# Kernel optimization log

Hardware: AMD Instinct MI355X
Metric: run time of the kernel (lower is better)

## Reference

```python
import jax, jax.numpy as jnp
import numpy as np

B, S, D, H, F = 8, 1024, 1024, 16, 4096
DH = D // H
LN_EPS = 1e-3  # keras LayerNormalization default


def layer_norm(x, g, b, eps=LN_EPS):
    m = jnp.mean(x, axis=-1, keepdims=True)
    v = jnp.mean(jnp.square(x - m), axis=-1, keepdims=True)
    return (x - m) * jax.lax.rsqrt(v + eps) * g + b


def setup_inputs() -> dict:
    key = jax.random.key(0)
    ks = jax.random.split(key, 16)
    s = 0.02
    return {
        "x": jax.random.normal(ks[0], (B, S, D), dtype=jnp.float32),
        "key_padding_mask": jax.random.randint(ks[1], (B, S), 0, 2) > 0,
        "wq": jax.random.normal(ks[2], (D, D), dtype=jnp.float32) * s,
        "wk": jax.random.normal(ks[3], (D, D), dtype=jnp.float32) * s,
        "wv": jax.random.normal(ks[4], (D, D), dtype=jnp.float32) * s,
        "wo": jax.random.normal(ks[5], (D, D), dtype=jnp.float32) * s,
        "gamma": jnp.ones((H,), dtype=jnp.float32),
        "ln_g": jnp.ones((3, D), dtype=jnp.float32),   # pre_attn, post_attn, pre_fc
        "ln_b": jnp.zeros((3, D), dtype=jnp.float32),
        "ln_fc_g": jnp.ones((F,), dtype=jnp.float32),  # post_fc_norm over fc_dim
        "ln_fc_b": jnp.zeros((F,), dtype=jnp.float32),
        "w1": jax.random.normal(ks[6], (D, F), dtype=jnp.float32) * s,
        "b1": jnp.zeros((F,), dtype=jnp.float32),
        "w2": jax.random.normal(ks[7], (F, D), dtype=jnp.float32) * s,
        "b2": jnp.zeros((D,), dtype=jnp.float32),
        "lam": jnp.ones((D,), dtype=jnp.float32),
    }


def reference(x, key_padding_mask, wq, wk, wv, wo, gamma, ln_g, ln_b,
              ln_fc_g, ln_fc_b, w1, b1, w2, b2, lam):
    # ---- attention sub-block (self-attention path, x_clt=None) ----
    residual = x
    h = layer_norm(x, ln_g[0], ln_b[0])                       # pre_attn_norm
    q = (h @ wq).reshape(B, S, H, DH)
    k = (h @ wk).reshape(B, S, H, DH)
    v = (h @ wv).reshape(B, S, H, DH)
    scores = jnp.einsum('bqhd,bkhd->bhqk', q, k) / jnp.sqrt(jnp.float32(DH))
    # key_padding_mask: True = masked key
    scores = jnp.where(key_padding_mask[:, None, None, :], -1e9, scores)
    v = jnp.where(key_padding_mask[:, :, None, None], 0.0, v)
    attn = jax.nn.softmax(scores, axis=-1)
    ws = jnp.einsum('bhqk,bkhd->bqhd', attn, v)
    ws = ws * gamma[None, None, :, None]                      # per-head scale
    out = ws.reshape(B, S, D) @ wo
    out = layer_norm(out, ln_g[1], ln_b[1])                   # post_attn_norm
    x = out + residual
    # ---- FFN sub-block ----
    residual = x
    h = layer_norm(x, ln_g[2], ln_b[2])                       # pre_fc_norm
    h = jax.nn.gelu(h @ w1 + b1, approximate=False)
    h = layer_norm(h, ln_fc_g, ln_fc_b)                       # post_fc_norm (fc_dim)
    h = h @ w2 + b2
    return h + residual * lam
```

## Files before the change

### kernel.cpp

```cpp
#include <hip/hip_runtime.h>
#include <math.h>

typedef _Float16 h_t;
typedef _Float16 h8 __attribute__((ext_vector_type(8)));
typedef _Float16 h4 __attribute__((ext_vector_type(4)));
typedef float    f4 __attribute__((ext_vector_type(4)));
typedef unsigned int u32;

#define SEQ   1024
#define DIM   1024
#define FDIM  4096
#define NB    8
#define NH    16
#define DHD   64
#define NROWS 8192

__device__ __forceinline__ void glds16(const void* g, void* l)
{
    __builtin_amdgcn_global_load_lds((const __attribute__((address_space(1))) u32*)g,
                                     (__attribute__((address_space(3))) u32*)l, 16, 0, 0);
}

__global__ __launch_bounds__(256)
void canon_mask_k(const void* __restrict__ raw, int* __restrict__ outm, int n)
{
    const unsigned int*  w  = (const unsigned int*)raw;
    const unsigned char* cb = (const unsigned char*)raw;
    __shared__ int flag;
    if (threadIdx.x == 0) flag = 0;
    __syncthreads();
    int bad = 0;
    for (int i = threadIdx.x; i < 1024; i += 256)
        if (w[i] > 1u) bad = 1;
    if (bad) flag = 1;
    __syncthreads();
    const bool is_i32 = (flag == 0);
    const int idx = blockIdx.x * 256 + threadIdx.x;
    if (idx < n) outm[idx] = is_i32 ? (w[idx] != 0u) : (cb[idx] != 0);
}

__global__ __launch_bounds__(256)
void wconv_k(const float* __restrict__ W, h_t* __restrict__ Wt, int K, int N)
{
    __shared__ float T[32][33];
    const int t  = threadIdx.x;
    const int k0 = blockIdx.y * 32, n0 = blockIdx.x * 32;
    const int r = t >> 3, c4 = (t & 7) * 4;
    const float4 v = *(const float4*)(W + (size_t)(k0 + r) * N + n0 + c4);
    T[r][c4 + 0] = v.x; T[r][c4 + 1] = v.y; T[r][c4 + 2] = v.z; T[r][c4 + 3] = v.w;
    __syncthreads();
    h4 o = { (h_t)T[c4 + 0][r], (h_t)T[c4 + 1][r], (h_t)T[c4 + 2][r], (h_t)T[c4 + 3][r] };
    *(h4*)(Wt + (size_t)(n0 + r) * K + k0 + c4) = o;
}

__device__ __forceinline__ void block_reduce2(float& s, float& ss)
{
    #pragma unroll
    for (int off = 32; off > 0; off >>= 1) {
        s  += __shfl_down(s,  off, 64);
        ss += __shfl_down(ss, off, 64);
    }
    __shared__ float sh[8];
    const int wid  = threadIdx.x >> 6;
    const int lane = threadIdx.x & 63;
    if (lane == 0) { sh[wid] = s; sh[4 + wid] = ss; }
    __syncthreads();
    s  = sh[0] + sh[1] + sh[2] + sh[3];
    ss = sh[4] + sh[5] + sh[6] + sh[7];
}

__global__ __launch_bounds__(256)
void ln1024_k(const float* __restrict__ in, const float* __restrict__ gw,
              const float* __restrict__ bw, h_t* __restrict__ out)
{
    const size_t base = (size_t)blockIdx.x * 1024;
    const int c = threadIdx.x * 4;
    float4 xv = *(const float4*)(in + base + c);
    float v[4] = {xv.x, xv.y, xv.z, xv.w};
    float s = v[0] + v[1] + v[2] + v[3];
    float ss = v[0]*v[0] + v[1]*v[1] + v[2]*v[2] + v[3]*v[3];
    block_reduce2(s, ss);
    const float mean = s * (1.f / 1024.f);
    const float rstd = rsqrtf(ss * (1.f / 1024.f) - mean * mean + 1e-3f);
    const float4 g4 = *(const float4*)(gw + c);
    const float4 b4 = *(const float4*)(bw + c);
    h4 oh = {(h_t)((v[0]-mean)*rstd*g4.x + b4.x), (h_t)((v[1]-mean)*rstd*g4.y + b4.y),
             (h_t)((v[2]-mean)*rstd*g4.z + b4.z), (h_t)((v[3]-mean)*rstd*g4.w + b4.w)};
    *(h4*)(out + base + c) = oh;
}

__global__ __launch_bounds__(256)
void ln_fuse_k(const h_t* __restrict__ proj, const float* __restrict__ x,
               const float* __restrict__ g1, const float* __restrict__ b1w,
               const float* __restrict__ g2, const float* __restrict__ b2w,
               h_t* __restrict__ x2out, h_t* __restrict__ h2out)
{
    const size_t base = (size_t)blockIdx.x * 1024;
    const int c = threadIdx.x * 4;
    h4 p = *(const h4*)(proj + base + c);
    float v[4] = {(float)p[0], (float)p[1], (float)p[2], (float)p[3]};
    float s = v[0]+v[1]+v[2]+v[3];
    float ss = v[0]*v[0]+v[1]*v[1]+v[2]*v[2]+v[3]*v[3];
    block_reduce2(s, ss);
    {
        const float mean = s * (1.f/1024.f);
        const float rstd = rsqrtf(ss * (1.f/1024.f) - mean*mean + 1e-3f);
        const float4 g4 = *(const float4*)(g1 + c);
        const float4 b4 = *(const float4*)(b1w + c);
        const float4 r4 = *(const float4*)(x + base + c);
        v[0] = (v[0]-mean)*rstd*g4.x + b4.x + r4.x;
        v[1] = (v[1]-mean)*rstd*g4.y + b4.y + r4.y;
        v[2] = (v[2]-mean)*rstd*g4.z + b4.z + r4.z;
        v[3] = (v[3]-mean)*rstd*g4.w + b4.w + r4.w;
    }
    h4 x2h = {(h_t)v[0], (h_t)v[1], (h_t)v[2], (h_t)v[3]};
    *(h4*)(x2out + base + c) = x2h;
    __syncthreads();
    float s2 = v[0]+v[1]+v[2]+v[3];
    float ss2 = v[0]*v[0]+v[1]*v[1]+v[2]*v[2]+v[3]*v[3];
    block_reduce2(s2, ss2);
    const float mean = s2 * (1.f/1024.f);
    const float rstd = rsqrtf(ss2 * (1.f/1024.f) - mean*mean + 1e-3f);
    const float4 g4 = *(const float4*)(g2 + c);
    const float4 b4 = *(const float4*)(b2w + c);
    h4 oh = {(h_t)((v[0]-mean)*rstd*g4.x + b4.x), (h_t)((v[1]-mean)*rstd*g4.y + b4.y),
             (h_t)((v[2]-mean)*rstd*g4.z + b4.z), (h_t)((v[3]-mean)*rstd*g4.w + b4.w)};
    *(h4*)(h2out + base + c) = oh;
}

__global__ __launch_bounds__(256)
void ln4096_k(h_t* __restrict__ buf, const float* __restrict__ gw,
              const float* __restrict__ bw)
{
    const size_t base = (size_t)blockIdx.x * 4096;
    const int t = threadIdx.x;
    float v[16];
    #pragma unroll
    for (int i = 0; i < 2; ++i) {
        h8 x = *(const h8*)(buf + base + (i * 256 + t) * 8);
        #pragma unroll
        for (int j = 0; j < 8; ++j) v[i * 8 + j] = (float)x[j];
    }
    float s = 0.f, ss = 0.f;
    #pragma unroll
    for (int i = 0; i < 16; ++i) { s += v[i]; ss += v[i] * v[i]; }
    block_reduce2(s, ss);
    const float mean = s * (1.f / 4096.f);
    const float rstd = rsqrtf(ss * (1.f / 4096.f) - mean * mean + 1e-3f);
    #pragma unroll
    for (int i = 0; i < 2; ++i) {
        const int c = (i * 256 + t) * 8;
        h8 o;
        #pragma unroll
        for (int j = 0; j < 8; ++j)
            o[j] = (h_t)((v[i*8+j] - mean) * rstd * gw[c + j] + bw[c + j]);
        *(h8*)(buf + base + c) = o;
    }
}

#define GEPI_QKV  0
#define GEPI_H16  2
#define GEPI_GELU 3
#define GEPI_FC2  4

__device__ __forceinline__ float gelu_exact(float x)
{
    return 0.5f * x * (1.f + erff(x * 0.70710678118654752440f));
}

template<int EPI>
__global__ __launch_bounds__(256, 2)
void hgemm_k(const h_t* __restrict__ A, const h_t* __restrict__ Wt,
             const float* __restrict__ bias, void* __restrict__ outv,
             int M, int K, int N,
             const int* __restrict__ mask, const h_t* __restrict__ resid,
             const float* __restrict__ lam, h_t* __restrict__ out2,
             h_t* __restrict__ out3)
{
    __shared__ h_t As[128 * 64];
    __shared__ h_t Bs[128 * 64];
    const int t = threadIdx.x;
    const int wv = t >> 6, lane = t & 63;

    int bx, by;
    {
        const int nwg = gridDim.x * gridDim.y;
        int wg = blockIdx.y * gridDim.x + blockIdx.x;
        const int xcd = wg & 7, rest = wg >> 3;
        const int q = nwg >> 3, r = nwg & 7;
        wg = (xcd < r ? xcd * (q + 1) : r * (q + 1) + (xcd - r) * q) + rest;
        bx = wg % gridDim.x; by = wg / gridDim.x;
    }
    const int m0 = by * 128, n0 = bx * 128;
    const int wr = (wv >> 1) * 64, wc = (wv & 1) * 64;
    const int lr = lane & 15, g = lane >> 4;
    const int sr = lane >> 3;
    const int sslot = (lane & 7) * 16;
    const int sswz = sr << 4;

    f4 acc[4][4] = {};

    for (int k0 = 0; k0 < K; k0 += 64) {
        __syncthreads();
        #pragma unroll
        for (int j = 0; j < 4; ++j) {
            const int r = j * 32 + wv * 8 + sr;
            glds16((const char*)A  + (((size_t)(m0 + r) * K + k0) << 1) + (sslot ^ sswz),
                   (char*)As + j * 4096 + wv * 1024);
            glds16((const char*)Wt + (((size_t)(n0 + r) * K + k0) << 1) + (sslot ^ sswz),
                   (char*)Bs + j * 4096 + wv * 1024);
        }
        __syncthreads();
        #pragma unroll
        for (int kk = 0; kk < 2; ++kk) {
            h8 af[4], bf[4];
            #pragma unroll
            for (int mt = 0; mt < 4; ++mt) {
                const int r = wr + mt * 16 + lr;
                af[mt] = *(const h8*)((const char*)As + r * 128 + ((kk * 64 + g * 16) ^ ((lr & 7) << 4)));
            }
            #pragma unroll
            for (int nt = 0; nt < 4; ++nt) {
                const int r = wc + nt * 16 + lr;
                bf[nt] = *(const h8*)((const char*)Bs + r * 128 + ((kk * 64 + g * 16) ^ ((lr & 7) << 4)));
            }
            #pragma unroll
            for (int mt = 0; mt < 4; ++mt)
                #pragma unroll
                for (int nt = 0; nt < 4; ++nt)
                    acc[mt][nt] = __builtin_amdgcn_mfma_f32_16x16x32_f16(af[mt], bf[nt], acc[mt][nt], 0, 0, 0);
        }
    }

    #pragma unroll
    for (int mt = 0; mt < 4; ++mt) {
        #pragma unroll
        for (int nt = 0; nt < 4; ++nt) {
            #pragma unroll
            for (int e = 0; e < 4; ++e) {
                const int row = m0 + wr + mt * 16 + g * 4 + e;
                const int col = n0 + wc + nt * 16 + lr;
                float val = acc[mt][nt][e];
                if constexpr (EPI == GEPI_QKV) {
                    const int matm = col >> 10;
                    const int cc = col & 1023;
                    const int b = row >> 10, s = row & 1023;
                    const int hh = cc >> 6, dd = cc & 63;
                    if (matm == 0)
                        ((h_t*)outv)[(((size_t)(b * NH + hh)) * SEQ + s) * DHD + dd] = (h_t)val;
                    else if (matm == 1)
                        out2[(((size_t)(b * NH + hh)) * SEQ + s) * DHD + dd] = (h_t)val;
                    else {
                        if (mask[row]) val = 0.f;
                        out3[(((size_t)(b * NH + hh)) * DHD + dd) * SEQ + s] = (h_t)val;
                    }
                } else if constexpr (EPI == GEPI_H16) {
                    ((h_t*)outv)[(size_t)row * N + col] = (h_t)val;
                } else if constexpr (EPI == GEPI_GELU) {
                    ((h_t*)outv)[(size_t)row * N + col] = (h_t)gelu_exact(val + bias[col]);
                } else {
                    val += bias[col] + (float)resid[(size_t)row * N + col] * lam[col];
                    ((float*)outv)[(size_t)row * N + col] = val;
                }
            }
        }
    }
}

__global__ __launch_bounds__(256, 3)
void attn_k(const h_t* __restrict__ Q, const h_t* __restrict__ K,
            const h_t* __restrict__ Vt, const int* __restrict__ mask,
            const float* __restrict__ gamma, h_t* __restrict__ out)
{
    __shared__ h_t Kt[64 * 64];
    __shared__ h_t Vs[64 * 64];
    __shared__ h_t Pl[4 * 16 * 64];
    __shared__ float madd[64];
    const int t = threadIdx.x, wv = t >> 6, lane = t & 63;
    const int lr = lane & 15, g = lane >> 4;
    const int b = blockIdx.z, h = blockIdx.y, q0 = blockIdx.x * 64;
    const size_t qkbase = ((size_t)(b * NH + h)) * SEQ * DHD;
    const size_t vbase  = ((size_t)(b * NH + h)) * DHD * SEQ;

    h8 qf[2];
    {
        const h_t* qp = Q + qkbase + (size_t)(q0 + wv * 16 + lr) * DHD;
        const h_t sc = (h_t)0.125f;
        qf[0] = *(const h8*)(qp + 8 * g) * sc;
        qf[1] = *(const h8*)(qp + 32 + 8 * g) * sc;
    }

    int koff[4][2], poff[4], paoff[2];
    #pragma unroll
    for (int tt = 0; tt < 4; ++tt) {
        const int r = tt * 16 + lr;
        const int sw = (r & 7) << 4;
        koff[tt][0] = r * 128 + ((g * 16) ^ sw);
        koff[tt][1] = r * 128 + ((64 + g * 16) ^ sw);
        poff[tt] = lr * 128 + (((tt * 32 + g * 8)) ^ ((lr & 7) << 4));
    }
    #pragma unroll
    for (int c = 0; c < 2; ++c)
        paoff[c] = lr * 128 + ((c * 64 + g * 16) ^ ((lr & 7) << 4));

    const int sgr = lane >> 3;
    const int sgslot = (lane & 7) * 16;
    const int sgswz = sgr << 4;

    f4 o[4] = {};
    float mrun = -3.0e38f, lrun = 0.f;
    h_t* pw = Pl + wv * 1024;

    for (int kt = 0; kt < SEQ / 64; ++kt) {
        const int kv0 = kt * 64;
        __syncthreads();
        #pragma unroll
        for (int i = 0; i < 2; ++i) {
            const int r = (wv * 2 + i) * 8 + sgr;
            glds16((const char*)K  + ((qkbase + (size_t)(kv0 + r) * DHD) << 1) + (sgslot ^ sgswz),
                   (char*)Kt + (wv * 2 + i) * 1024);
            glds16((const char*)Vt + ((vbase + (size_t)r * SEQ + kv0) << 1) + (sgslot ^ sgswz),
                   (char*)Vs + (wv * 2 + i) * 1024);
        }
        if (t < 64) madd[t] = mask[b * SEQ + kv0 + t] ? -1e9f : 0.f;
        __syncthreads();

        f4 s[4] = {};
        #pragma unroll
        for (int tt = 0; tt < 4; ++tt)
            #pragma unroll
            for (int c = 0; c < 2; ++c) {
                h8 kf = *(const h8*)((const char*)Kt + koff[tt][c]);
                s[tt] = __builtin_amdgcn_mfma_f32_16x16x32_f16(kf, qf[c], s[tt], 0, 0, 0);
            }
        float mt_ = -3.0e38f;
        #pragma unroll
        for (int tt = 0; tt < 4; ++tt) {
            f4 ma = *(const f4*)(&madd[tt * 16 + g * 4]);
            s[tt] += ma;
            mt_ = fmaxf(mt_, fmaxf(fmaxf(s[tt][0], s[tt][1]), fmaxf(s[tt][2], s[tt][3])));
        }
        mt_ = fmaxf(mt_, __shfl_xor(mt_, 16, 64));
        mt_ = fmaxf(mt_, __shfl_xor(mt_, 32, 64));

        const bool skip = __all(mt_ <= mrun + 8.f);
        float scl = 1.f;
        if (!skip) {
            const float mnew = fmaxf(mrun, mt_);
            scl = __expf(mrun - mnew);
            mrun = mnew;
        }
        float ps = 0.f;
        #pragma unroll
        for (int tt = 0; tt < 4; ++tt) {
            const float p0 = __expf(s[tt][0] - mrun), p1 = __expf(s[tt][1] - mrun);
            const float p2 = __expf(s[tt][2] - mrun), p3 = __expf(s[tt][3] - mrun);
            ps += p0 + p1 + p2 + p3;
            h4 pq = {(h_t)p0, (h_t)p1, (h_t)p2, (h_t)p3};
            *(h4*)((char*)pw + poff[tt]) = pq;
        }
        ps += __shfl_xor(ps, 16, 64);
        ps += __shfl_xor(ps, 32, 64);
        if (skip) {
            lrun += ps;
        } else {
            lrun = lrun * scl + ps;
            #pragma unroll
            for (int e = 0; e < 4; ++e) {
                const float sce = __shfl(scl, g * 4 + e, 64);
                #pragma unroll
                for (int dt = 0; dt < 4; ++dt) o[dt][e] *= sce;
            }
        }
        #pragma unroll
        for (int c = 0; c < 2; ++c) {
            h8 pa = *(const h8*)((const char*)pw + paoff[c]);
            #pragma unroll
            for (int dt = 0; dt < 4; ++dt) {
                h8 vf = *(const h8*)((const char*)Vs + koff[dt][c]);
                o[dt] = __builtin_amdgcn_mfma_f32_16x16x32_f16(pa, vf, o[dt], 0, 0, 0);
            }
        }
    }
    const float gm = gamma[h];
    #pragma unroll
    for (int e = 0; e < 4; ++e) {
        const float inv = gm / __shfl(lrun, g * 4 + e, 64);
        const int row = q0 + wv * 16 + g * 4 + e;
        #pragma unroll
        for (int dt = 0; dt < 4; ++dt)
            out[(size_t)(b * SEQ + row) * DIM + h * DHD + dt * 16 + lr] = (h_t)(o[dt][e] * inv);
    }
}

extern "C" void kernel_launch(void* const* d_in, const int* in_sizes, int n_in,
                              void* d_out, int out_size, void* d_ws, size_t ws_size,
                              hipStream_t stream)
{
    const float* x       = (const float*)d_in[0];
    const void*  kpm     = d_in[1];
    const float* wq      = (const float*)d_in[2];
    const float* wk      = (const float*)d_in[3];
    const float* wv      = (const float*)d_in[4];
    const float* wo      = (const float*)d_in[5];
    const float* gamma   = (const float*)d_in[6];
    const float* ln_g    = (const float*)d_in[7];
    const float* ln_b    = (const float*)d_in[8];
    const float* ln_fc_g = (const float*)d_in[9];
    const float* ln_fc_b = (const float*)d_in[10];
    const float* w1      = (const float*)d_in[11];
    const float* b1      = (const float*)d_in[12];
    const float* w2      = (const float*)d_in[13];
    const float* b2      = (const float*)d_in[14];
    const float* lam     = (const float*)d_in[15];
    float* out = (float*)d_out;

    char* ws = (char*)d_ws;
    const size_t MB = 1 << 20;
    int* mask_i = (int*)ws;
    h_t* wqkvt = (h_t*)(ws + 1  * MB);
    h_t* wqt = wqkvt;
    h_t* wkt = wqkvt + (size_t)1024 * 1024;
    h_t* wvt = wqkvt + (size_t)2048 * 1024;
    h_t* wot = (h_t*)(ws + 7  * MB);
    h_t* w1t = (h_t*)(ws + 9  * MB);
    h_t* w2t = (h_t*)(ws + 17 * MB);
    h_t* bufA = (h_t*)(ws + 25 * MB);
    h_t* bufQ = (h_t*)(ws + 41 * MB);
    h_t* bufK = (h_t*)(ws + 57 * MB);
    h_t* bufV = (h_t*)(ws + 73 * MB);
    h_t* bufX2 = (h_t*)(ws + 89 * MB);

    canon_mask_k<<<NROWS / 256, 256, 0, stream>>>(kpm, mask_i, NROWS);

    wconv_k<<<dim3(32, 32),  256, 0, stream>>>(wq, wqt, DIM, DIM);
    wconv_k<<<dim3(32, 32),  256, 0, stream>>>(wk, wkt, DIM, DIM);
    wconv_k<<<dim3(32, 32),  256, 0, stream>>>(wv, wvt, DIM, DIM);
    wconv_k<<<dim3(32, 32),  256, 0, stream>>>(wo, wot, DIM, DIM);
    wconv_k<<<dim3(128, 32), 256, 0, stream>>>(w1, w1t, DIM, FDIM);
    wconv_k<<<dim3(32, 128), 256, 0, stream>>>(w2, w2t, FDIM, DIM);

    ln1024_k<<<NROWS, 256, 0, stream>>>(x, ln_g, ln_b, bufA);

    hgemm_k<GEPI_QKV><<<dim3(3072 / 128, NROWS / 128), 256, 0, stream>>>(
        bufA, wqkvt, nullptr, bufQ, NROWS, DIM, 3072, mask_i, nullptr, nullptr, bufK, bufV);

    attn_k<<<dim3(SEQ / 64, NH, NB), 256, 0, stream>>>(bufQ, bufK, bufV, mask_i, gamma, bufA);

    hgemm_k<GEPI_H16><<<dim3(DIM / 128, NROWS / 128), 256, 0, stream>>>(
        bufA, wot, nullptr, bufQ, NROWS, DIM, DIM, nullptr, nullptr, nullptr, nullptr, nullptr);

    ln_fuse_k<<<NROWS, 256, 0, stream>>>(bufQ, x, ln_g + DIM, ln_b + DIM,
                                         ln_g + 2 * DIM, ln_b + 2 * DIM, bufX2, bufA);

    const int CH = 4096;
    for (int c = 0; c < NROWS / CH; ++c) {
        const size_t ro = (size_t)c * CH;
        hgemm_k<GEPI_GELU><<<dim3(FDIM / 128, CH / 128), 256, 0, stream>>>(
            bufA + ro * DIM, w1t, b1, bufK, CH, DIM, FDIM, nullptr, nullptr, nullptr, nullptr, nullptr);
        ln4096_k<<<CH, 256, 0, stream>>>(bufK, ln_fc_g, ln_fc_b);
        hgemm_k<GEPI_FC2><<<dim3(DIM / 128, CH / 128), 256, 0, stream>>>(
            bufK, w2t, b2, out + ro * DIM, CH, FDIM, DIM, nullptr, bufX2 + ro * DIM, lam, nullptr, nullptr);
    }
}
```

Baseline: 637.6 us.

## Double-buffer GEMM LDS tiles and merge square weight conversions into one launch

The fp16 MFMA GEMM now holds two LDS buffers for the A and B tiles. It issues the global-to-LDS loads for the next K tile right after the barrier, so they run while MFMAs work on the current tile, and it drops one barrier per iteration. This is meant to hide global load latency behind compute, at the cost of doubling LDS use to 64KB per block, which may limit occupancy. Separately, the four DIM×DIM weight transpose/convert launches are merged into one 3D-grid kernel to cut launch overhead.

```diff
diff --git a/kernel.cpp b/kernel.cpp
--- a/kernel.cpp
+++ b/kernel.cpp
@@ -39,18 +39,36 @@
     if (idx < n) outm[idx] = is_i32 ? (w[idx] != 0u) : (cb[idx] != 0);
 }
 
-__global__ __launch_bounds__(256)
-void wconv_k(const float* __restrict__ W, h_t* __restrict__ Wt, int K, int N)
+__device__ __forceinline__ void wconv_body(const float* __restrict__ W, h_t* __restrict__ Wt,
+                                           int K, int N, int bx, int by)
 {
     __shared__ float T[32][33];
     const int t  = threadIdx.x;
-    const int k0 = blockIdx.y * 32, n0 = blockIdx.x * 32;
+    const int k0 = by * 32, n0 = bx * 32;
     const int r = t >> 3, c4 = (t & 7) * 4;
     const float4 v = *(const float4*)(W + (size_t)(k0 + r) * N + n0 + c4);
     T[r][c4 + 0] = v.x; T[r][c4 + 1] = v.y; T[r][c4 + 2] = v.z; T[r][c4 + 3] = v.w;
     __syncthreads();
     h4 o = { (h_t)T[c4 + 0][r], (h_t)T[c4 + 1][r], (h_t)T[c4 + 2][r], (h_t)T[c4 + 3][r] };
     *(h4*)(Wt + (size_t)(n0 + r) * K + k0 + c4) = o;
+}
+
+__global__ __launch_bounds__(256)
+void wconv_k(const float* __restrict__ W, h_t* __restrict__ Wt, int K, int N)
+{
+    wconv_body(W, Wt, K, N, blockIdx.x, blockIdx.y);
+}
+
+__global__ __launch_bounds__(256)
+void wconv4_k(const float* __restrict__ W0, const float* __restrict__ W1,
+              const float* __restrict__ W2, const float* __restrict__ W3,
+              h_t* __restrict__ O0, h_t* __restrict__ O1,
+              h_t* __restrict__ O2, h_t* __restrict__ O3)
+{
+    const int z = blockIdx.z;
+    const float* W = (z == 0) ? W0 : (z == 1) ? W1 : (z == 2) ? W2 : W3;
+    h_t*       Wt = (z == 0) ? O0 : (z == 1) ? O1 : (z == 2) ? O2 : O3;
+    wconv_body(W, Wt, DIM, DIM, blockIdx.x, blockIdx.y);
 }
 
 __device__ __forceinline__ void block_reduce2(float& s, float& ss)
@@ -177,8 +195,8 @@
              const float* __restrict__ lam, h_t* __restrict__ out2,
              h_t* __restrict__ out3)
 {
-    __shared__ h_t As[128 * 64];
-    __shared__ h_t Bs[128 * 64];
+    __shared__ h_t As[2][128 * 64];
+    __shared__ h_t Bs[2][128 * 64];
     const int t = threadIdx.x;
     const int wv = t >> 6, lane = t & 63;
 
@@ -198,31 +216,36 @@
     const int sslot = (lane & 7) * 16;
     const int sswz = sr << 4;
 
-    f4 acc[4][4] = {};
-
-    for (int k0 = 0; k0 < K; k0 += 64) {
-        __syncthreads();
+    auto STAGE = [&](int which, int k0) {
         #pragma unroll
         for (int j = 0; j < 4; ++j) {
             const int r = j * 32 + wv * 8 + sr;
             glds16((const char*)A  + (((size_t)(m0 + r) * K + k0) << 1) + (sslot ^ sswz),
-                   (char*)As + j * 4096 + wv * 1024);
+                   (char*)As[which] + j * 4096 + wv * 1024);
             glds16((const char*)Wt + (((size_t)(n0 + r) * K + k0) << 1) + (sslot ^ sswz),
-                   (char*)Bs + j * 4096 + wv * 1024);
-        }
+                   (char*)Bs[which] + j * 4096 + wv * 1024);
+        }
+    };
+
+    f4 acc[4][4] = {};
+
+    STAGE(0, 0);
+    int cur = 0;
+    for (int k0 = 0; k0 < K; k0 += 64) {
         __syncthreads();
+        if (k0 + 64 < K) STAGE(cur ^ 1, k0 + 64);
         #pragma unroll
         for (int kk = 0; kk < 2; ++kk) {
             h8 af[4], bf[4];
             #pragma unroll
             for (int mt = 0; mt < 4; ++mt) {
                 const int r = wr + mt * 16 + lr;
-                af[mt] = *(const h8*)((const char*)As + r * 128 + ((kk * 64 + g * 16) ^ ((lr & 7) << 4)));
+                af[mt] = *(const h8*)((const char*)As[cur] + r * 128 + ((kk * 64 + g * 16) ^ ((lr & 7) << 4)));
             }
             #pragma unroll
             for (int nt = 0; nt < 4; ++nt) {
                 const int r = wc + nt * 16 + lr;
-                bf[nt] = *(const h8*)((const char*)Bs + r * 128 + ((kk * 64 + g * 16) ^ ((lr & 7) << 4)));
+                bf[nt] = *(const h8*)((const char*)Bs[cur] + r * 128 + ((kk * 64 + g * 16) ^ ((lr & 7) << 4)));
             }
             #pragma unroll
             for (int mt = 0; mt < 4; ++mt)
@@ -230,6 +253,7 @@
                 for (int nt = 0; nt < 4; ++nt)
                     acc[mt][nt] = __builtin_amdgcn_mfma_f32_16x16x32_f16(af[mt], bf[nt], acc[mt][nt], 0, 0, 0);
         }
+        cur ^= 1;
     }
 
     #pragma unroll
@@ -433,10 +457,7 @@
 
     canon_mask_k<<<NROWS / 256, 256, 0, stream>>>(kpm, mask_i, NROWS);
 
-    wconv_k<<<dim3(32, 32),  256, 0, stream>>>(wq, wqt, DIM, DIM);
-    wconv_k<<<dim3(32, 32),  256, 0, stream>>>(wk, wkt, DIM, DIM);
-    wconv_k<<<dim3(32, 32),  256, 0, stream>>>(wv, wvt, DIM, DIM);
-    wconv_k<<<dim3(32, 32),  256, 0, stream>>>(wo, wot, DIM, DIM);
+    wconv4_k<<<dim3(32, 32, 4), 256, 0, stream>>>(wq, wk, wv, wo, wqt, wkt, wvt, wot);
     wconv_k<<<dim3(128, 32), 256, 0, stream>>>(w1, w1t, DIM, FDIM);
     wconv_k<<<dim3(32, 128), 256, 0, stream>>>(w2, w2t, FDIM, DIM);
 
```

After: 625.9 us. No clear change (-1.8%).
